# Optimization experiments

Measured on AMD Instinct MI355X. Metric: run time of the kernel, lower is better.

Reference implementation:

```python
import jax, jax.numpy as jnp
import numpy as np
import math

H, NH, LAT = 2048, 16, 512
D = H // NH  # head_dim = 128
B, S = 2, 2048


def setup_inputs() -> dict:
    key = jax.random.key(0)
    ks = jax.random.split(key, 18)
    w = lambda k, i, o: jax.random.normal(k, (i, o), dtype=jnp.float32) * 0.02
    inp = {
        'hidden_states': jax.random.normal(ks[0], (B, S, H), dtype=jnp.float32),
        'attention_mask': jnp.ones((B, S), dtype=jnp.int32),
        'W_DKV': w(ks[1], H, LAT), 'b_DKV': jnp.zeros((LAT,), jnp.float32),
        'W_DQ': w(ks[2], H, LAT), 'b_DQ': jnp.zeros((LAT,), jnp.float32),
        'W_UK': w(ks[3], LAT, H), 'b_UK': jnp.zeros((H,), jnp.float32),
        'W_UV': w(ks[4], LAT, H), 'b_UV': jnp.zeros((H,), jnp.float32),
        'W_UQ': w(ks[5], LAT, H), 'b_UQ': jnp.zeros((H,), jnp.float32),
        'W_KR': w(ks[6], H, D), 'b_KR': jnp.zeros((D,), jnp.float32),
        'W_QR': w(ks[7], H, D), 'b_QR': jnp.zeros((D,), jnp.float32),
        'W_O': w(ks[8], H, H), 'b_O': jnp.zeros((H,), jnp.float32),
    }
    return inp


def _rope(x, seq_len):
    # x: [B, S, D]; rotate-half RoPE exactly as the torch module
    half = D // 2
    inv_freq = 1.0 / (10000.0 ** (jnp.arange(0, D, 2, dtype=jnp.float32) / D))
    ang = jnp.arange(seq_len, dtype=jnp.float32)[:, None] * inv_freq[None, :]  # [S, half]
    sin, cos = jnp.sin(ang), jnp.cos(ang)
    x1, x2 = x[..., :half], x[..., half:]
    return jnp.concatenate([x1 * cos - x2 * sin, x1 * sin + x2 * cos], axis=-1)


def reference(hidden_states, attention_mask, W_DKV, b_DKV, W_DQ, b_DQ,
              W_UK, b_UK, W_UV, b_UV, W_UQ, b_UQ,
              W_KR, b_KR, W_QR, b_QR, W_O, b_O):
    b, s, _ = hidden_states.shape
    c_kv = hidden_states @ W_DKV + b_DKV          # [B,S,LAT]
    c_q = hidden_states @ W_DQ + b_DQ
    k_c = (c_kv @ W_UK + b_UK).reshape(b, s, NH, D).transpose(0, 2, 1, 3)  # [B,H,S,D]
    v_c = (c_kv @ W_UV + b_UV).reshape(b, s, NH, D).transpose(0, 2, 1, 3)
    q_c = (c_q @ W_UQ + b_UQ).reshape(b, s, NH, D).transpose(0, 2, 1, 3)
    k_r = _rope(hidden_states @ W_KR + b_KR, s)[:, None]  # [B,1,S,D] shared across heads
    q_r = _rope(hidden_states @ W_QR + b_QR, s)[:, None]
    scale = 1.0 / math.sqrt(D)
    # q·k with concatenated [compressed | rope] head layout, decomposed to avoid materializing cat
    scores = (jnp.einsum('bhqd,bhkd->bhqk', q_c, k_c)
              + jnp.einsum('bhqd,bhkd->bhqk', q_r, k_r)) * scale  # [B,H,S,S]
    mask = attention_mask[:, None, None, :]
    scores = jnp.where(mask == 0, -jnp.inf, scores)
    attn = jax.nn.softmax(scores, axis=-1)
    ctx = jnp.einsum('bhqk,bhkd->bhqd', attn, v_c)
    ctx = ctx.transpose(0, 2, 1, 3).reshape(b, s, H)
    return ctx @ W_O + b_O
```

## Files before the change

### kernel.cpp

```cpp
#include <hip/hip_runtime.h>
#include <hip/hip_bf16.h>
#include <stdint.h>

typedef __hip_bfloat16 bf16;
typedef __attribute__((ext_vector_type(8))) short s8v;
typedef __attribute__((ext_vector_type(4))) float f4v;
typedef __attribute__((ext_vector_type(16))) float f16v;

__device__ __forceinline__ void gld16(const bf16* g, bf16* l) {
  __builtin_amdgcn_global_load_lds(
      (__attribute__((address_space(1))) unsigned int*)g,
      (__attribute__((address_space(3))) unsigned int*)l, 16, 0, 0);
}

__device__ __forceinline__ f4v mfma16(s8v a, s8v b, f4v c) {
  return __builtin_amdgcn_mfma_f32_16x16x32_bf16(a, b, c, 0, 0, 0);
}

__device__ __forceinline__ f16v mfma32(s8v a, s8v b, f16v c) {
  return __builtin_amdgcn_mfma_f32_32x32x16_bf16(a, b, c, 0, 0, 0);
}

__device__ __forceinline__ unsigned short f2bfu(float f) {
  union { bf16 h; unsigned short u; } cv;
  cv.h = __float2bfloat16(f);
  return cv.u;
}

__global__ __launch_bounds__(256) void prep(
    const float* __restrict__ hs, bf16* __restrict__ hsb,
    const float* __restrict__ bdkv, const float* __restrict__ bdq,
    const float* __restrict__ bkr, const float* __restrict__ bqr,
    float* __restrict__ bcat,
    const float* __restrict__ wdkv, bf16* __restrict__ tdkv,
    const float* __restrict__ wdq,  bf16* __restrict__ tdq,
    const float* __restrict__ wkr,  bf16* __restrict__ tkr,
    const float* __restrict__ wqr,  bf16* __restrict__ tqr,
    const float* __restrict__ wuk,  bf16* __restrict__ tuk,
    const float* __restrict__ wuv,  bf16* __restrict__ tuv,
    const float* __restrict__ wuq,  bf16* __restrict__ tuq,
    const float* __restrict__ wo,   bf16* __restrict__ to_) {
  int bid = blockIdx.x;
  int tid = threadIdx.x;
  if (bid < 4096) {
    int i = (bid * 256 + tid) * 8;
    union { s8v v; unsigned short u[8]; } pk;
#pragma unroll
    for (int j = 0; j < 8; j++) pk.u[j] = f2bfu(hs[i + j]);
    *(s8v*)(hsb + i) = pk.v;
    return;
  }
  if (bid == 4096) {
#pragma unroll
    for (int p = 0; p < 5; p++) {
      int i = tid + p * 256;
      float v;
      if (i < 512)       v = bdkv[i];
      else if (i < 1024) v = bdq[i - 512];
      else if (i < 1152) v = bkr[i - 1024];
      else               v = bqr[i - 1152];
      bcat[i] = v;
    }
    return;
  }
  bid -= 4097;
  const float* src; bf16* dst; int R, C;
  if      (bid < 1024) { src = wdkv; dst = tdkv; R = 2048; C = 512;  }
  else if (bid < 2048) { src = wdq;  dst = tdq;  R = 2048; C = 512;  bid -= 1024; }
  else if (bid < 2304) { src = wkr;  dst = tkr;  R = 2048; C = 128;  bid -= 2048; }
  else if (bid < 2560) { src = wqr;  dst = tqr;  R = 2048; C = 128;  bid -= 2304; }
  else if (bid < 3584) { src = wuk;  dst = tuk;  R = 512;  C = 2048; bid -= 2560; }
  else if (bid < 4608) { src = wuv;  dst = tuv;  R = 512;  C = 2048; bid -= 3584; }
  else if (bid < 5632) { src = wuq;  dst = tuq;  R = 512;  C = 2048; bid -= 4608; }
  else                 { src = wo;   dst = to_;  R = 2048; C = 2048; bid -= 5632; }
  __shared__ float t[32][33];
  int C32 = C >> 5;
  int bx = bid % C32, by = bid / C32;
  int tx = tid & 31, ty = tid >> 5;
  int c0 = bx * 32, r0 = by * 32;
#pragma unroll
  for (int i = 0; i < 32; i += 8)
    t[ty + i][tx] = src[(size_t)(r0 + ty + i) * C + c0 + tx];
  __syncthreads();
#pragma unroll
  for (int i = 0; i < 32; i += 8)
    dst[(size_t)(c0 + ty + i) * R + r0 + tx] = __float2bfloat16(t[tx][ty + i]);
}

__global__ void rope_kernel(const bf16* __restrict__ inK, bf16* __restrict__ outK,
                            const bf16* __restrict__ inQ, bf16* __restrict__ outQ) {
  const bf16* in = (blockIdx.y == 0) ? inK : inQ;
  bf16* out = (blockIdx.y == 0) ? outK : outQ;
  int row = blockIdx.x;
  int d = threadIdx.x;
  int pos = row & 2047;
  float x1 = __bfloat162float(in[(size_t)row * 128 + d]);
  float x2 = __bfloat162float(in[(size_t)row * 128 + 64 + d]);
  float inv = exp2f(-(float)d * (13.287712379549449f / 64.0f));
  float ang = (float)pos * inv;
  float sn = sinf(ang), cs = cosf(ang);
  out[(size_t)row * 128 + d]      = __float2bfloat16(x1 * cs - x2 * sn);
  out[(size_t)row * 128 + 64 + d] = __float2bfloat16(x1 * sn + x2 * cs);
}

template <int MODE>
__global__ __launch_bounds__(256) void gemm_bt(
    const bf16* __restrict__ A, const bf16* __restrict__ A2,
    const bf16* __restrict__ Bt,
    const float* __restrict__ b0, const float* __restrict__ b1,
    const float* __restrict__ b2,
    void* __restrict__ C0, void* __restrict__ C1,
    void* __restrict__ C2, void* __restrict__ C3,
    int M, int N, int K) {
  __shared__ bf16 sA[128 * 32];
  __shared__ bf16 sB[128 * 32];
  __shared__ bf16 trb[(MODE == 2) ? 4 * 64 * 72 : 1];
  const int tid = threadIdx.x, lane = tid & 63, wid = tid >> 6;
  const int l15 = lane & 15, l4 = lane >> 4;
  const int m0 = blockIdx.y * 128, n0 = blockIdx.x * 128;
  const int wm = (wid >> 1) * 64, wn = (wid & 1) * 64;
  f4v acc[4][4] = {};
  const bf16* Ause = (MODE == 2 && n0 >= 4096) ? A2 : A;
  const bf16* gA = Ause + (size_t)m0 * K;
  const bf16* gB = Bt + (size_t)n0 * K;
  const int row = tid >> 2, col = (tid & 3) * 8;
  for (int k0 = 0; k0 < K; k0 += 32) {
    gld16(gA + (size_t)row * K + k0 + col,        sA + tid * 8);
    gld16(gA + (size_t)(row + 64) * K + k0 + col, sA + (tid + 256) * 8);
    gld16(gB + (size_t)row * K + k0 + col,        sB + tid * 8);
    gld16(gB + (size_t)(row + 64) * K + k0 + col, sB + (tid + 256) * 8);
    __syncthreads();
    s8v a[4], b[4];
#pragma unroll
    for (int i = 0; i < 4; i++) a[i] = *(const s8v*)(sA + (wm + i * 16 + l15) * 32 + l4 * 8);
#pragma unroll
    for (int j = 0; j < 4; j++) b[j] = *(const s8v*)(sB + (wn + j * 16 + l15) * 32 + l4 * 8);
#pragma unroll
    for (int i = 0; i < 4; i++)
#pragma unroll
      for (int j = 0; j < 4; j++) acc[i][j] = mfma16(a[i], b[j], acc[i][j]);
    __syncthreads();
  }
  if (MODE == 2 && n0 >= 2048 && n0 < 4096) {
    bf16* tb = trb + wid * (64 * 72);
    const int nn0 = n0 - 2048;
    const int hh = nn0 >> 7;
    const int bb = m0 >> 11;
    const int ss0 = (m0 & 2047) + wm;
#pragma unroll
    for (int j = 0; j < 4; j++) {
      const float bv = b1[nn0 + wn + j * 16 + l15];
#pragma unroll
      for (int i = 0; i < 4; i++) {
        uint2 w;
        w.x = (unsigned int)f2bfu(acc[i][j][0] + bv) | ((unsigned int)f2bfu(acc[i][j][1] + bv) << 16);
        w.y = (unsigned int)f2bfu(acc[i][j][2] + bv) | ((unsigned int)f2bfu(acc[i][j][3] + bv) << 16);
        *(uint2*)(tb + (j * 16 + l15) * 72 + i * 16 + l4 * 4) = w;
      }
    }
    asm volatile("s_waitcnt lgkmcnt(0)" ::: "memory");
    __builtin_amdgcn_sched_barrier(0);
    const int dl = lane >> 3, sl = (lane & 7) * 8;
    bf16* dstbase = (bf16*)C1 +
        ((size_t)(bb * 16 + hh) * 128 + wn) * 2048 + ss0;
#pragma unroll
    for (int r = 0; r < 8; r++) {
      int d_rel = r * 8 + dl;
      s8v v = *(const s8v*)(tb + d_rel * 72 + sl);
      *(s8v*)(dstbase + (size_t)d_rel * 2048 + sl) = v;
    }
    return;
  }
#pragma unroll
  for (int j = 0; j < 4; j++) {
    const int nb = n0 + wn + j * 16;
    const int n = nb + l15;
    if (MODE == 3) {
      const float bv = b0[n];
#pragma unroll
      for (int i = 0; i < 4; i++) {
        size_t mb = m0 + wm + i * 16 + l4 * 4;
#pragma unroll
        for (int g = 0; g < 4; g++)
          ((float*)C0)[(mb + g) * (size_t)N + n] = acc[i][j][g] + bv;
      }
    } else if (MODE == 1) {
      const float bv = b0[n];
      bf16* dst; int stride, nc;
      if (nb < 512)       { dst = (bf16*)C0; stride = 512; nc = n; }
      else if (nb < 1024) { dst = (bf16*)C1; stride = 512; nc = n - 512; }
      else if (nb < 1152) { dst = (bf16*)C2; stride = 128; nc = n - 1024; }
      else                { dst = (bf16*)C3; stride = 128; nc = n - 1152; }
#pragma unroll
      for (int i = 0; i < 4; i++) {
        size_t mb = m0 + wm + i * 16 + l4 * 4;
#pragma unroll
        for (int g = 0; g < 4; g++)
          dst[(mb + g) * (size_t)stride + nc] = __float2bfloat16(acc[i][j][g] + bv);
      }
    } else {
      if (nb < 2048) {
        const float bv = b0[n];
        bf16* dst = (bf16*)C0;
#pragma unroll
        for (int i = 0; i < 4; i++) {
          size_t mb = m0 + wm + i * 16 + l4 * 4;
#pragma unroll
          for (int g = 0; g < 4; g++)
            dst[(mb + g) * (size_t)2048 + n] = __float2bfloat16(acc[i][j][g] + bv);
        }
      } else {
        const float bv = b2[n - 4096];
        bf16* dst = (bf16*)C2;
        int nn = n - 4096;
#pragma unroll
        for (int i = 0; i < 4; i++) {
          size_t mb = m0 + wm + i * 16 + l4 * 4;
#pragma unroll
          for (int g = 0; g < 4; g++)
            dst[(mb + g) * (size_t)2048 + nn] = __float2bfloat16(acc[i][j][g] + bv);
        }
      }
    }
  }
}

__global__ __launch_bounds__(256, 2) void flash_attn(
    const bf16* __restrict__ Qc, const bf16* __restrict__ Kc,
    const bf16* __restrict__ Qr, const bf16* __restrict__ Kr,
    const bf16* __restrict__ VT, const int* __restrict__ amask,
    bf16* __restrict__ ctx) {
  const int S = 2048, H = 2048, D = 128;
  __shared__ bf16 sK[3][16 * 32 * 8];
  __shared__ bf16 sKr[3][16 * 32 * 8];
  __shared__ bf16 sVT[3][4 * 128 * 8];

  const int tid = threadIdx.x, lane = tid & 63, wid = tid >> 6;
  const int l31 = lane & 31, hi = lane >> 5;
  const int phys = blockIdx.x + 16 * blockIdx.y;
  const int lid  = (phys & 7) * 64 + (phys >> 3);
  const int qt = lid & 15, bh = lid >> 4;
  const int b = bh >> 4, h = bh & 15;
  const size_t bS = (size_t)b * S;
  const int q0 = qt * 128 + wid * 32;

  s8v qcf[8], qrf[8];
  {
    const bf16* pc = Qc + (bS + q0 + l31) * H + h * D + hi * 8;
    const bf16* pr = Qr + (bS + q0 + l31) * D + hi * 8;
#pragma unroll
    for (int t = 0; t < 8; t++) {
      qcf[t] = *(const s8v*)(pc + t * 16);
      qrf[t] = *(const s8v*)(pr + t * 16);
    }
  }

  f16v oacc[4] = {};
  float lsum = 0.f;
  const float scl = 0.08838834764831845f;

  auto stage = [&](int buf, int kv) {
#pragma unroll
    for (int p = 0; p < 2; p++) {
      int idx = tid + p * 256;
      int key = (idx & 31), dch = (idx >> 5);
      gld16(Kc + (bS + kv + key) * H + h * D + dch * 8, sK[buf] + idx * 8);
      gld16(Kr + (bS + kv + key) * D + dch * 8, sKr[buf] + idx * 8);
      int d = (idx & 127), kch = (idx >> 7);
      gld16(VT + ((size_t)bh * D + d) * S + kv + kch * 8, sVT[buf] + idx * 8);
    }
  };

  const int xaddr = (lane ^ 32) * 4;

  int4 mvC[4], mvN[4];
  stage(0, 0);
#pragma unroll
  for (int g2 = 0; g2 < 4; g2++)
    mvC[g2] = *(const int4*)(amask + bS + 8 * g2 + 4 * hi);
  stage(1, 32);

  for (int it = 0; it < 64; ++it) {
    const int cur = it % 3;
    const int kv0 = it * 32;
    if (it < 63) asm volatile("s_waitcnt vmcnt(10)" ::: "memory");
    else         asm volatile("s_waitcnt vmcnt(0)" ::: "memory");
    __builtin_amdgcn_s_barrier();
    __builtin_amdgcn_sched_barrier(0);

    if (it + 1 < 64) {
#pragma unroll
      for (int g2 = 0; g2 < 4; g2++)
        mvN[g2] = *(const int4*)(amask + bS + kv0 + 32 + 8 * g2 + 4 * hi);
    } else {
#pragma unroll
      for (int g2 = 0; g2 < 4; g2++) mvN[g2] = mvC[g2];
    }
    if (it + 2 < 64) stage((it + 2) % 3, kv0 + 64);

    f16v scc = {}, scr = {};
    __builtin_amdgcn_s_setprio(1);
#pragma unroll
    for (int t = 0; t < 8; t++) {
      s8v kf = *(const s8v*)(sK[cur] + ((2 * t + hi) * 32 + l31) * 8);
      scc = mfma32(kf, qcf[t], scc);
      s8v rf = *(const s8v*)(sKr[cur] + ((2 * t + hi) * 32 + l31) * 8);
      scr = mfma32(rf, qrf[t], scr);
    }
    __builtin_amdgcn_s_setprio(0);

    unsigned int pk2[4][2];
#pragma unroll
    for (int g2 = 0; g2 < 4; g2++) {
      const int* mm = (const int*)&mvC[g2];
#pragma unroll
      for (int w = 0; w < 2; w++) {
        int r = 4 * g2 + 2 * w;
        float pa = mm[2 * w]     ? __expf((scc[r] + scr[r]) * scl) : 0.f;
        float pb = mm[2 * w + 1] ? __expf((scc[r + 1] + scr[r + 1]) * scl) : 0.f;
        lsum += pa + pb;
        pk2[g2][w] = (unsigned int)f2bfu(pa) | ((unsigned int)f2bfu(pb) << 16);
      }
    }

    s8v pf[2];
#pragma unroll
    for (int ks = 0; ks < 2; ks++) {
      int passA = hi ? (int)pk2[2 * ks][0] : (int)pk2[2 * ks + 1][0];
      int passB = hi ? (int)pk2[2 * ks][1] : (int)pk2[2 * ks + 1][1];
      int recvA = __builtin_amdgcn_ds_bpermute(xaddr, passA);
      int recvB = __builtin_amdgcn_ds_bpermute(xaddr, passB);
      union { int w[4]; s8v v; } u;
      u.w[0] = hi ? recvA : (int)pk2[2 * ks][0];
      u.w[1] = hi ? recvB : (int)pk2[2 * ks][1];
      u.w[2] = hi ? (int)pk2[2 * ks + 1][0] : recvA;
      u.w[3] = hi ? (int)pk2[2 * ks + 1][1] : recvB;
      pf[ks] = u.v;
    }

    __builtin_amdgcn_s_setprio(1);
#pragma unroll
    for (int dblk = 0; dblk < 4; dblk++) {
      s8v vf0 = *(const s8v*)(sVT[cur] + ((0 + hi) * 128 + dblk * 32 + l31) * 8);
      oacc[dblk] = mfma32(pf[0], vf0, oacc[dblk]);
      s8v vf1 = *(const s8v*)(sVT[cur] + ((2 + hi) * 128 + dblk * 32 + l31) * 8);
      oacc[dblk] = mfma32(pf[1], vf1, oacc[dblk]);
    }
    __builtin_amdgcn_s_setprio(0);

#pragma unroll
    for (int g2 = 0; g2 < 4; g2++) mvC[g2] = mvN[g2];
  }

  float s = lsum;
  s += __shfl_xor(s, 32, 64);
  float inv[16];
#pragma unroll
  for (int g = 0; g < 16; g++) {
    int ql = (g & 3) + 8 * (g >> 2) + 4 * hi;
    inv[g] = 1.0f / __shfl(s, ql, 64);
  }

#pragma unroll
  for (int dblk = 0; dblk < 4; dblk++)
#pragma unroll
    for (int g = 0; g < 16; g++) {
      int qrow = q0 + (g & 3) + 8 * (g >> 2) + 4 * hi;
      ctx[(bS + qrow) * H + h * D + dblk * 32 + l31] =
          __float2bfloat16(oacc[dblk][g] * inv[g]);
    }
}

extern "C" void kernel_launch(void* const* d_in, const int* in_sizes, int n_in,
                              void* d_out, int out_size, void* d_ws, size_t ws_size,
                              hipStream_t stream) {
  const float* hs    = (const float*)d_in[0];
  const int*   amask = (const int*)d_in[1];
  const float* W_DKV = (const float*)d_in[2];  const float* b_DKV = (const float*)d_in[3];
  const float* W_DQ  = (const float*)d_in[4];  const float* b_DQ  = (const float*)d_in[5];
  const float* W_UK  = (const float*)d_in[6];  const float* b_UK  = (const float*)d_in[7];
  const float* W_UV  = (const float*)d_in[8];  const float* b_UV  = (const float*)d_in[9];
  const float* W_UQ  = (const float*)d_in[10]; const float* b_UQ  = (const float*)d_in[11];
  const float* W_KR  = (const float*)d_in[12]; const float* b_KR  = (const float*)d_in[13];
  const float* W_QR  = (const float*)d_in[14]; const float* b_QR  = (const float*)d_in[15];
  const float* W_O   = (const float*)d_in[16]; const float* b_O   = (const float*)d_in[17];

  char* wsb = (char*)d_ws;
  size_t off = 0;
  auto allocB = [&](size_t bytes) {
    void* p = wsb + off; off = (off + bytes + 255) & ~(size_t)255; return p;
  };
  float* bcat  = (float*)allocB(1280 * 4);
  bf16* hsb    = (bf16*)allocB((size_t)4096 * 2048 * 2);
  bf16* wt_dkv = (bf16*)allocB((size_t)512 * 2048 * 2);
  bf16* wt_dq  = (bf16*)allocB((size_t)512 * 2048 * 2);
  bf16* wt_kr  = (bf16*)allocB((size_t)128 * 2048 * 2);
  bf16* wt_qr  = (bf16*)allocB((size_t)128 * 2048 * 2);
  bf16* wt_uk  = (bf16*)allocB((size_t)2048 * 512 * 2);
  bf16* wt_uv  = (bf16*)allocB((size_t)2048 * 512 * 2);
  bf16* wt_uq  = (bf16*)allocB((size_t)2048 * 512 * 2);
  bf16* wt_o   = (bf16*)allocB((size_t)2048 * 2048 * 2);
  bf16* c_kv   = (bf16*)allocB((size_t)4096 * 512 * 2);
  bf16* c_q    = (bf16*)allocB((size_t)4096 * 512 * 2);
  bf16* krl    = (bf16*)allocB((size_t)4096 * 128 * 2);
  bf16* qrl    = (bf16*)allocB((size_t)4096 * 128 * 2);
  bf16* k_r    = (bf16*)allocB((size_t)4096 * 128 * 2);
  bf16* q_r    = (bf16*)allocB((size_t)4096 * 128 * 2);
  bf16* k_c    = (bf16*)allocB((size_t)4096 * 2048 * 2);
  bf16* q_c    = (bf16*)allocB((size_t)4096 * 2048 * 2);
  bf16* vT     = (bf16*)allocB((size_t)4096 * 2048 * 2);
  bf16* ctx    = (bf16*)allocB((size_t)4096 * 2048 * 2);
  (void)wt_uv; (void)wt_uq;

  prep<<<13825, 256, 0, stream>>>(hs, hsb,
      b_DKV, b_DQ, b_KR, b_QR, bcat,
      W_DKV, wt_dkv, W_DQ, wt_dq, W_KR, wt_kr, W_QR, wt_qr,
      W_UK, wt_uk, W_UV, wt_uv, W_UQ, wt_uq, W_O, wt_o);

  gemm_bt<1><<<dim3(10, 32), 256, 0, stream>>>(
      hsb, nullptr, wt_dkv, bcat, nullptr, nullptr,
      c_kv, c_q, krl, qrl, 4096, 1280, 2048);
  rope_kernel<<<dim3(4096, 2), 64, 0, stream>>>(krl, k_r, qrl, q_r);

  gemm_bt<2><<<dim3(48, 32), 256, 0, stream>>>(
      c_kv, c_q, wt_uk, b_UK, b_UV, b_UQ,
      k_c, vT, q_c, nullptr, 4096, 6144, 512);

  flash_attn<<<dim3(16, 32), 256, 0, stream>>>(q_c, k_c, q_r, k_r, vT, amask, ctx);

  gemm_bt<3><<<dim3(16, 32), 256, 0, stream>>>(
      ctx, nullptr, wt_o, b_O, nullptr, nullptr,
      d_out, nullptr, nullptr, nullptr, 4096, 2048, 2048);
}
```

Before: 442.9 us.

## Add narrow-N GEMM tiles and XCD-aware block remapping

The GEMM kernel gains a template parameter for the N tile width. The first projection GEMM (N=1280) now uses 128x64 tiles, doubling its block count from 320 to 640 so work spreads more evenly across the CUs. All GEMMs also remap the linear block id so that consecutive tiles are grouped onto the same XCD, aiming to improve L2 reuse of shared A/B panels. In exchange, the narrower tiles cut per-block arithmetic intensity and reload the A operand more often.

```diff
diff --git a/kernel.cpp b/kernel.cpp
--- a/kernel.cpp
+++ b/kernel.cpp
@@ -103,7 +103,7 @@
   out[(size_t)row * 128 + 64 + d] = __float2bfloat16(x1 * sn + x2 * cs);
 }
 
-template <int MODE>
+template <int MODE, int NT>
 __global__ __launch_bounds__(256) void gemm_bt(
     const bf16* __restrict__ A, const bf16* __restrict__ A2,
     const bf16* __restrict__ Bt,
@@ -112,14 +112,19 @@
     void* __restrict__ C0, void* __restrict__ C1,
     void* __restrict__ C2, void* __restrict__ C3,
     int M, int N, int K) {
+  constexpr int WN = NT / 2;
+  constexpr int NJ = WN / 16;
   __shared__ bf16 sA[128 * 32];
-  __shared__ bf16 sB[128 * 32];
+  __shared__ bf16 sB[NT * 32];
   __shared__ bf16 trb[(MODE == 2) ? 4 * 64 * 72 : 1];
   const int tid = threadIdx.x, lane = tid & 63, wid = tid >> 6;
   const int l15 = lane & 15, l4 = lane >> 4;
-  const int m0 = blockIdx.y * 128, n0 = blockIdx.x * 128;
-  const int wm = (wid >> 1) * 64, wn = (wid & 1) * 64;
-  f4v acc[4][4] = {};
+  const int nwg = gridDim.x * gridDim.y;
+  int bid = blockIdx.x + gridDim.x * blockIdx.y;
+  bid = (bid & 7) * (nwg >> 3) + (bid >> 3);
+  const int m0 = (bid / gridDim.x) * 128, n0 = (bid % gridDim.x) * NT;
+  const int wm = (wid >> 1) * 64, wn = (wid & 1) * WN;
+  f4v acc[4][NJ] = {};
   const bf16* Ause = (MODE == 2 && n0 >= 4096) ? A2 : A;
   const bf16* gA = Ause + (size_t)m0 * K;
   const bf16* gB = Bt + (size_t)n0 * K;
@@ -128,17 +133,18 @@
     gld16(gA + (size_t)row * K + k0 + col,        sA + tid * 8);
     gld16(gA + (size_t)(row + 64) * K + k0 + col, sA + (tid + 256) * 8);
     gld16(gB + (size_t)row * K + k0 + col,        sB + tid * 8);
-    gld16(gB + (size_t)(row + 64) * K + k0 + col, sB + (tid + 256) * 8);
+    if (NT == 128)
+      gld16(gB + (size_t)(row + 64) * K + k0 + col, sB + (tid + 256) * 8);
     __syncthreads();
-    s8v a[4], b[4];
+    s8v a[4], b[NJ];
 #pragma unroll
     for (int i = 0; i < 4; i++) a[i] = *(const s8v*)(sA + (wm + i * 16 + l15) * 32 + l4 * 8);
 #pragma unroll
-    for (int j = 0; j < 4; j++) b[j] = *(const s8v*)(sB + (wn + j * 16 + l15) * 32 + l4 * 8);
+    for (int j = 0; j < NJ; j++) b[j] = *(const s8v*)(sB + (wn + j * 16 + l15) * 32 + l4 * 8);
 #pragma unroll
     for (int i = 0; i < 4; i++)
 #pragma unroll
-      for (int j = 0; j < 4; j++) acc[i][j] = mfma16(a[i], b[j], acc[i][j]);
+      for (int j = 0; j < NJ; j++) acc[i][j] = mfma16(a[i], b[j], acc[i][j]);
     __syncthreads();
   }
   if (MODE == 2 && n0 >= 2048 && n0 < 4096) {
@@ -148,7 +154,7 @@
     const int bb = m0 >> 11;
     const int ss0 = (m0 & 2047) + wm;
 #pragma unroll
-    for (int j = 0; j < 4; j++) {
+    for (int j = 0; j < NJ; j++) {
       const float bv = b1[nn0 + wn + j * 16 + l15];
 #pragma unroll
       for (int i = 0; i < 4; i++) {
@@ -172,7 +178,7 @@
     return;
   }
 #pragma unroll
-  for (int j = 0; j < 4; j++) {
+  for (int j = 0; j < NJ; j++) {
     const int nb = n0 + wn + j * 16;
     const int n = nb + l15;
     if (MODE == 3) {
@@ -417,18 +423,18 @@
       W_DKV, wt_dkv, W_DQ, wt_dq, W_KR, wt_kr, W_QR, wt_qr,
       W_UK, wt_uk, W_UV, wt_uv, W_UQ, wt_uq, W_O, wt_o);
 
-  gemm_bt<1><<<dim3(10, 32), 256, 0, stream>>>(
+  gemm_bt<1, 64><<<dim3(20, 32), 256, 0, stream>>>(
       hsb, nullptr, wt_dkv, bcat, nullptr, nullptr,
       c_kv, c_q, krl, qrl, 4096, 1280, 2048);
   rope_kernel<<<dim3(4096, 2), 64, 0, stream>>>(krl, k_r, qrl, q_r);
 
-  gemm_bt<2><<<dim3(48, 32), 256, 0, stream>>>(
+  gemm_bt<2, 128><<<dim3(48, 32), 256, 0, stream>>>(
       c_kv, c_q, wt_uk, b_UK, b_UV, b_UQ,
       k_c, vT, q_c, nullptr, 4096, 6144, 512);
 
   flash_attn<<<dim3(16, 32), 256, 0, stream>>>(q_c, k_c, q_r, k_r, vT, amask, ctx);
 
-  gemm_bt<3><<<dim3(16, 32), 256, 0, stream>>>(
+  gemm_bt<3, 128><<<dim3(16, 32), 256, 0, stream>>>(
       ctx, nullptr, wt_o, b_O, nullptr, nullptr,
       d_out, nullptr, nullptr, nullptr, 4096, 2048, 2048);
 }
```

Result: faster. 430.7 us (-2.7%).
